# Kernel optimization log

Measured on AMD Instinct MI355X. Metric: run time of the kernel, lower is better.

The kernel has to match this reference:

```python
import jax, jax.numpy as jnp
import numpy as np

N_NODES = 100000
N_EDGES = 3200000
D_FEAT = 64
H_SIZE = 32
N_CLASSES = 10


def setup_inputs() -> dict:
    key = jax.random.key(0)
    ks = jax.random.split(key, 9)
    x = jax.random.normal(ks[0], (N_NODES, D_FEAT), dtype=jnp.float32)
    edge_index = jax.random.randint(ks[1], (2, N_EDGES), 0, N_NODES, dtype=jnp.int64)
    y = jax.random.randint(ks[2], (N_NODES,), 0, N_CLASSES, dtype=jnp.int64)
    s1 = 1.0 / np.sqrt(D_FEAT)
    s2 = 1.0 / np.sqrt(H_SIZE)
    W1_rel = jax.random.uniform(ks[3], (H_SIZE, D_FEAT), jnp.float32, -s1, s1)
    b1_rel = jax.random.uniform(ks[4], (H_SIZE,), jnp.float32, -s1, s1)
    W1_root = jax.random.uniform(ks[5], (H_SIZE, D_FEAT), jnp.float32, -s1, s1)
    W2_rel = jax.random.uniform(ks[6], (N_CLASSES, H_SIZE), jnp.float32, -s2, s2)
    b2_rel = jax.random.uniform(ks[7], (N_CLASSES,), jnp.float32, -s2, s2)
    W2_root = jax.random.uniform(ks[8], (N_CLASSES, H_SIZE), jnp.float32, -s2, s2)
    return {"x": x, "edge_index": edge_index, "y": y,
            "W1_rel": W1_rel, "b1_rel": b1_rel, "W1_root": W1_root,
            "W2_rel": W2_rel, "b2_rel": b2_rel, "W2_root": W2_root}


def _graph_conv(x, src, dst, W_rel, b_rel, W_root):
    # PyG GraphConv (aggr='add'): out_i = W_root x_i + b + W_rel * sum_{j: (j->i)} x_j
    agg = jax.ops.segment_sum(x[src], dst, num_segments=N_NODES)  # [N, d_in]
    return agg @ W_rel.T + b_rel + x @ W_root.T


def reference(x, edge_index, y, W1_rel, b1_rel, W1_root, W2_rel, b2_rel, W2_root):
    src, dst = edge_index[0], edge_index[1]
    h = jax.nn.relu(_graph_conv(x, src, dst, W1_rel, b1_rel, W1_root))  # [N, 32]
    logits = _graph_conv(h, src, dst, W2_rel, b2_rel, W2_root)          # [N, 10]
    logp = jax.nn.log_softmax(logits, axis=-1)
    loss = -jnp.mean(jnp.take_along_axis(logp, y[:, None], axis=-1)[:, 0])
    return loss
```

## Files before the change

### kernel.cpp

```cpp
#include <hip/hip_runtime.h>
#include <hip/hip_bf16.h>
#include <hip/hip_fp8.h>

#define D_FEAT 64
#define H_SIZE 32
#define N_CLASSES 10
#define NPB 256
#define MAXB 512
#define NCHUNK 256
#define BT 1024
#define NT 256

using short8 = __attribute__((ext_vector_type(8))) short;
using f32x4v = __attribute__((ext_vector_type(4))) float;

__device__ inline short f2bf(float f) {
    __hip_bfloat16 h = __float2bfloat16(f);
    return *reinterpret_cast<short*>(&h);
}


__global__ __launch_bounds__(NT) void dense1_mfma(
    const float* __restrict__ x, const float* __restrict__ W1_rel,
    const float* __restrict__ b1, const float* __restrict__ W1_root,
    unsigned* __restrict__ xr8, float* __restrict__ xroot, int n_nodes) {
    __shared__ unsigned short sW[64 * 72];
    __shared__ float sOut[64 * 65];
    __shared__ float sb[H_SIZE];
    int tid = threadIdx.x;
    for (int i = tid; i < 64 * 64; i += NT) {
        int n = i >> 6, k = i & 63;
        float w = (n < 32) ? W1_rel[n * 64 + k] : W1_root[(n - 32) * 64 + k];
        sW[n * 72 + k] = (unsigned short)f2bf(w);
    }
    if (tid < H_SIZE) sb[tid] = b1[tid];
    __syncthreads();

    int lane = tid & 63, wave = tid >> 6;
    int r16 = lane & 15, h = lane >> 4;

    short8 bf[4][2];
#pragma unroll
    for (int t = 0; t < 4; ++t)
#pragma unroll
        for (int s = 0; s < 2; ++s) {
            const unsigned short* p = &sW[(t * 16 + r16) * 72 + s * 32 + h * 8];
            bf[t][s] = *reinterpret_cast<const short8*>(p);
        }

    int nbase = blockIdx.x * 64 + wave * 16;
    int row = nbase + r16;
    int rowc = min(row, n_nodes - 1);

    short8 af[2];
#pragma unroll
    for (int s = 0; s < 2; ++s) {
        const float* px = x + (size_t)rowc * D_FEAT + s * 32 + h * 8;
        float4 lo = *reinterpret_cast<const float4*>(px);
        float4 hi = *reinterpret_cast<const float4*>(px + 4);
        short8 a;
        a[0] = f2bf(lo.x); a[1] = f2bf(lo.y); a[2] = f2bf(lo.z); a[3] = f2bf(lo.w);
        a[4] = f2bf(hi.x); a[5] = f2bf(hi.y); a[6] = f2bf(hi.z); a[7] = f2bf(hi.w);
        af[s] = a;
    }

    f32x4v acc[4] = {{0.f,0.f,0.f,0.f},{0.f,0.f,0.f,0.f},
                     {0.f,0.f,0.f,0.f},{0.f,0.f,0.f,0.f}};
#pragma unroll
    for (int t = 0; t < 4; ++t) {
        acc[t] = __builtin_amdgcn_mfma_f32_16x16x32_bf16(af[0], bf[t][0], acc[t], 0, 0, 0);
        acc[t] = __builtin_amdgcn_mfma_f32_16x16x32_bf16(af[1], bf[t][1], acc[t], 0, 0, 0);
    }
#pragma unroll
    for (int t = 0; t < 4; ++t)
#pragma unroll
        for (int r = 0; r < 4; ++r)
            sOut[(wave * 16 + h * 4 + r) * 65 + t * 16 + r16] = acc[t][r];
    __syncthreads();

    int nl = lane;
    int g = blockIdx.x * 64 + nl;
    if (g < n_nodes) {
        if (wave < 2) {
            unsigned w4[4];
#pragma unroll
            for (int q = 0; q < 4; ++q) {
                unsigned wd = 0;
#pragma unroll
                for (int b = 0; b < 4; ++b) {
                    float v = sOut[nl * 65 + wave * 16 + q * 4 + b];
                    __hip_fp8_e4m3 f8(v);
                    wd |= ((unsigned)f8.__x) << (8 * b);
                }
                w4[q] = wd;
            }
            *reinterpret_cast<uint4*>(&xr8[(size_t)g * 8 + wave * 4]) =
                make_uint4(w4[0], w4[1], w4[2], w4[3]);
        } else {
            int co = (wave - 2) * 16;
#pragma unroll
            for (int q = 0; q < 4; ++q) {
                float4 v;
                v.x = sOut[nl * 65 + 32 + co + q * 4 + 0] + sb[co + q * 4 + 0];
                v.y = sOut[nl * 65 + 32 + co + q * 4 + 1] + sb[co + q * 4 + 1];
                v.z = sOut[nl * 65 + 32 + co + q * 4 + 2] + sb[co + q * 4 + 2];
                v.w = sOut[nl * 65 + 32 + co + q * 4 + 3] + sb[co + q * 4 + 3];
                *reinterpret_cast<float4*>(&xroot[(size_t)g * 32 + co + q * 4]) = v;
            }
        }
    }
}


__global__ __launch_bounds__(BT) void bucket_count(
    const int* __restrict__ dst, int* __restrict__ counts,
    int n_edges, int nbuckets, int ept) {
    __shared__ int hist[MAXB];
    for (int i = threadIdx.x; i < nbuckets; i += BT) hist[i] = 0;
    __syncthreads();
    int beg = blockIdx.x * ept;
    int end = min(beg + ept, n_edges);
    for (int e = beg + threadIdx.x; e < end; e += BT)
        atomicAdd(&hist[dst[e] >> 8], 1);
    __syncthreads();
    for (int b = threadIdx.x; b < nbuckets; b += BT)
        counts[b * NCHUNK + blockIdx.x] = hist[b];
}

__global__ __launch_bounds__(NPB) void bucket_totals(
    const int* __restrict__ counts, int* __restrict__ totals) {
    int b = blockIdx.x, tid = threadIdx.x;
    int v = counts[b * NCHUNK + tid];
#pragma unroll
    for (int o = 32; o > 0; o >>= 1) v += __shfl_down(v, o, 64);
    __shared__ int part[NPB / 64];
    if ((tid & 63) == 0) part[tid >> 6] = v;
    __syncthreads();
    if (tid == 0) {
        int s = 0;
#pragma unroll
        for (int w = 0; w < NPB / 64; ++w) s += part[w];
        totals[b] = s;
    }
}

__global__ __launch_bounds__(MAXB) void scan_small(
    const int* __restrict__ totals, int* __restrict__ bbase, int nbuckets) {
    __shared__ int lds[MAXB];
    int tid = threadIdx.x;
    int v = (tid < nbuckets) ? totals[tid] : 0;
    lds[tid] = v;
    __syncthreads();
    for (int off = 1; off < MAXB; off <<= 1) {
        int t = (tid >= off) ? lds[tid - off] : 0;
        __syncthreads();
        lds[tid] += t;
        __syncthreads();
    }
    if (tid < nbuckets) bbase[tid] = lds[tid] - v;
}

__global__ __launch_bounds__(NPB) void scan_within(
    int* __restrict__ counts, const int* __restrict__ bbase) {
    __shared__ int lds[NPB];
    int b = blockIdx.x, tid = threadIdx.x;
    int v = counts[b * NCHUNK + tid];
    lds[tid] = v;
    __syncthreads();
    for (int off = 1; off < NPB; off <<= 1) {
        int t = (tid >= off) ? lds[tid - off] : 0;
        __syncthreads();
        lds[tid] += t;
        __syncthreads();
    }
    counts[b * NCHUNK + tid] = bbase[b] + lds[tid] - v;
}

__global__ __launch_bounds__(BT) void bucket_scatter(
    const int* __restrict__ src, const int* __restrict__ dst,
    const int* __restrict__ base, unsigned* __restrict__ packed,
    int n_edges, int nbuckets, int ept) {
    __shared__ int cur[MAXB];
    for (int b = threadIdx.x; b < nbuckets; b += BT)
        cur[b] = base[b * NCHUNK + blockIdx.x];
    __syncthreads();
    int beg = blockIdx.x * ept;
    int end = min(beg + ept, n_edges);
    for (int e = beg + threadIdx.x; e < end; e += BT) {
        int s = src[e], d = dst[e];
        int slot = atomicAdd(&cur[d >> 8], 1);
        packed[slot] = (unsigned)s | ((unsigned)(d & 255) << 24);
    }
}


__global__ __launch_bounds__(NPB) void csr_build(
    const unsigned* __restrict__ packed, const int* __restrict__ base,
    int* __restrict__ rowptr, int* __restrict__ csr,
    int n_nodes, int nbuckets, int n_edges) {
    __shared__ int cnt[NPB];
    __shared__ int cur[NPB];
    int b = blockIdx.x, tid = threadIdx.x;
    int pBeg = base[b * NCHUNK];
    int pEnd = (b + 1 < nbuckets) ? base[(b + 1) * NCHUNK] : n_edges;
    cnt[tid] = 0;
    __syncthreads();
    for (int i = pBeg + tid; i < pEnd; i += NPB)
        atomicAdd(&cnt[packed[i] >> 24], 1);
    __syncthreads();
    int v = cnt[tid];
    cur[tid] = v;
    __syncthreads();
    for (int off = 1; off < NPB; off <<= 1) {
        int t = (tid >= off) ? cur[tid - off] : 0;
        __syncthreads();
        cur[tid] += t;
        __syncthreads();
    }
    int gbase = pBeg + cur[tid] - v;
    int n = (b << 8) + tid;
    if (n < n_nodes) rowptr[n] = gbase;
    if (b == nbuckets - 1 && tid == 0) rowptr[n_nodes] = n_edges;
    cur[tid] = gbase;
    __syncthreads();
    for (int i = pBeg + tid; i < pEnd; i += NPB) {
        unsigned p = packed[i];
        int slot = atomicAdd(&cur[p >> 24], 1);
        csr[slot] = (int)(p & 0xFFFFFF);
    }
}


__global__ __launch_bounds__(NT) void gather1_kernel(
    const unsigned* __restrict__ xr8, const float* __restrict__ xroot,
    const int* __restrict__ rowptr, const int* __restrict__ csr,
    const float* __restrict__ W2_rel, const float* __restrict__ b2,
    const float* __restrict__ W2_root,
    __hip_bfloat16* __restrict__ h2, float* __restrict__ hroot, int n_nodes) {
    __shared__ float sWrelT[H_SIZE * 17];
    __shared__ float sWrootT[H_SIZE * 17];
    __shared__ float sb[16];
    __shared__ float sh[32][33];
    int tid = threadIdx.x;
    for (int i = tid; i < H_SIZE * 17; i += NT) { sWrelT[i] = 0.f; sWrootT[i] = 0.f; }
    __syncthreads();
    for (int i = tid; i < N_CLASSES * H_SIZE; i += NT) {
        int c = i >> 5, j = i & 31;
        sWrelT[j * 17 + c] = W2_rel[i];
        sWrootT[j * 17 + c] = W2_root[i];
    }
    if (tid < 16) sb[tid] = (tid < N_CLASSES) ? b2[tid] : 0.f;

    int t = blockIdx.x * NT + tid;
    int n = t >> 3, c2 = t & 7;
    float a0 = 0.f, a1 = 0.f, a2 = 0.f, a3 = 0.f;
    if (n < n_nodes) {
        int beg = rowptr[n], end = rowptr[n + 1];
        int nfull = (end - beg) & ~7;
        int i = beg;
        for (; i < beg + nfull; i += 8) {
            int e = csr[i + c2];
#pragma unroll
            for (int j = 0; j < 8; ++j) {
                int s = __shfl(e, j, 8);
                unsigned p = xr8[(size_t)s * 8 + c2];
                __hip_fp8_e4m3 f0, f1, f2, f3;
                f0.__x = (unsigned char)(p & 0xff);
                f1.__x = (unsigned char)((p >> 8) & 0xff);
                f2.__x = (unsigned char)((p >> 16) & 0xff);
                f3.__x = (unsigned char)(p >> 24);
                a0 += (float)f0; a1 += (float)f1; a2 += (float)f2; a3 += (float)f3;
            }
        }
        if (i < end) {
            int cnt = end - i;
            int e = csr[i + ((c2 < cnt) ? c2 : cnt - 1)];
#pragma unroll
            for (int j = 0; j < 8; ++j) {
                int s = __shfl(e, j, 8);
                unsigned p = xr8[(size_t)s * 8 + c2];
                if (j < cnt) {
                    __hip_fp8_e4m3 f0, f1, f2, f3;
                    f0.__x = (unsigned char)(p & 0xff);
                    f1.__x = (unsigned char)((p >> 8) & 0xff);
                    f2.__x = (unsigned char)((p >> 16) & 0xff);
                    f3.__x = (unsigned char)(p >> 24);
                    a0 += (float)f0; a1 += (float)f1; a2 += (float)f2; a3 += (float)f3;
                }
            }
        }
        float4 xr4 = *reinterpret_cast<const float4*>(&xroot[(size_t)n * 32 + c2 * 4]);
        a0 = fmaxf(a0 + xr4.x, 0.f);
        a1 = fmaxf(a1 + xr4.y, 0.f);
        a2 = fmaxf(a2 + xr4.z, 0.f);
        a3 = fmaxf(a3 + xr4.w, 0.f);
    }
    int nl = tid >> 3;
    sh[nl][c2 * 4 + 0] = a0;
    sh[nl][c2 * 4 + 1] = a1;
    sh[nl][c2 * 4 + 2] = a2;
    sh[nl][c2 * 4 + 3] = a3;
    __syncthreads();

#pragma unroll
    for (int pass = 0; pass < 2; ++pass) {
        int idx = pass * NT + tid;
        int nl2 = idx >> 4, c = idx & 15;
        int n2 = blockIdx.x * 32 + nl2;
        if (n2 < n_nodes) {
            float ar = 0.f, ao = 0.f;
#pragma unroll
            for (int j = 0; j < H_SIZE; ++j) {
                float hv = sh[nl2][j];
                ar += hv * sWrelT[j * 17 + c];
                ao += hv * sWrootT[j * 17 + c];
            }
            h2[(size_t)n2 * 16 + c] = __float2bfloat16(ar);
            hroot[(size_t)n2 * 16 + c] = ao + sb[c];
        }
    }
}


__global__ __launch_bounds__(NT) void gather2_loss_kernel(
    const unsigned* __restrict__ h2u,
    const float* __restrict__ hroot,
    const int* __restrict__ rowptr, const int* __restrict__ csr,
    const int* __restrict__ y, float* __restrict__ loss,
    int n_nodes, float invN) {
    int t = blockIdx.x * NT + threadIdx.x;
    int n = t >> 3, c2 = t & 7;
    int lane = threadIdx.x & 63;
    bool active = (n < n_nodes);

    float a0 = 0.f, a1 = 0.f;
    int yv = 0;
    if (active) {
        int beg = rowptr[n], end = rowptr[n + 1];
        int nfull = (end - beg) & ~7;
        int i = beg;
        for (; i < beg + nfull; i += 8) {
            int e = csr[i + c2];
#pragma unroll
            for (int j = 0; j < 8; ++j) {
                int s = __shfl(e, j, 8);
                unsigned p = h2u[(size_t)s * 8 + c2];
                a0 += __uint_as_float(p << 16);
                a1 += __uint_as_float(p & 0xFFFF0000u);
            }
        }
        if (i < end) {
            int cnt = end - i;
            int e = csr[i + ((c2 < cnt) ? c2 : cnt - 1)];
#pragma unroll
            for (int j = 0; j < 8; ++j) {
                int s = __shfl(e, j, 8);
                unsigned p = h2u[(size_t)s * 8 + c2];
                if (j < cnt) {
                    a0 += __uint_as_float(p << 16);
                    a1 += __uint_as_float(p & 0xFFFF0000u);
                }
            }
        }
        float2 hr = ((const float2*)hroot)[(size_t)n * 8 + c2];
        a0 += hr.x; a1 += hr.y;
        yv = y[n];
    }
    bool cv = active && (c2 < 5);
    float lm = cv ? fmaxf(a0, a1) : -INFINITY;
#pragma unroll
    for (int m = 1; m < 8; m <<= 1) lm = fmaxf(lm, __shfl_xor(lm, m, 64));
    float es = cv ? (expf(a0 - lm) + expf(a1 - lm)) : 0.f;
#pragma unroll
    for (int m = 1; m < 8; m <<= 1) es += __shfl_xor(es, m, 64);
    int srcl = (lane & ~7) + (yv >> 1);
    float ly0 = __shfl(a0, srcl, 64);
    float ly1 = __shfl(a1, srcl, 64);
    float ly = (yv & 1) ? ly1 : ly0;
    float contrib = (active && c2 == 0) ? (lm + logf(es) - ly) * invN : 0.f;

#pragma unroll
    for (int o = 32; o > 0; o >>= 1) contrib += __shfl_down(contrib, o, 64);
    __shared__ float part[NT / 64];
    if (lane == 0) part[threadIdx.x >> 6] = contrib;
    __syncthreads();
    if (threadIdx.x == 0) {
        float v = 0.f;
#pragma unroll
        for (int w = 0; w < NT / 64; ++w) v += part[w];
        atomicAdd(loss, v);
    }
}


extern "C" void kernel_launch(void* const* d_in, const int* in_sizes, int n_in,
                              void* d_out, int out_size, void* d_ws, size_t ws_size,
                              hipStream_t stream) {
    const float* x       = (const float*)d_in[0];
    const int*   ei      = (const int*)d_in[1];
    const int*   y       = (const int*)d_in[2];
    const float* W1_rel  = (const float*)d_in[3];
    const float* b1_rel  = (const float*)d_in[4];
    const float* W1_root = (const float*)d_in[5];
    const float* W2_rel  = (const float*)d_in[6];
    const float* b2_rel  = (const float*)d_in[7];
    const float* W2_root = (const float*)d_in[8];
    float* loss = (float*)d_out;

    const int n_nodes = in_sizes[0] / D_FEAT;
    const int n_edges = in_sizes[1] / 2;
    const int* src = ei;
    const int* dst = ei + n_edges;

    const int nbuckets = (n_nodes + NPB - 1) / NPB;
    const int M = nbuckets * NCHUNK;
    const int ept = (n_edges + NCHUNK - 1) / NCHUNK;

    size_t off = 0;
    auto alloc = [&](size_t bytes) {
        void* p = (char*)d_ws + off;
        off = (off + bytes + 255) & ~(size_t)255;
        return p;
    };
    int*            counts = (int*)alloc((size_t)(M + 1) * 4);
    int*            totals = (int*)alloc((size_t)MAXB * 4);
    int*            bbase  = (int*)alloc((size_t)MAXB * 4);
    unsigned*       packed = (unsigned*)alloc((size_t)n_edges * 4);
    int*            rowptr = (int*)alloc((size_t)(n_nodes + 1) * 4);
    int*            csr    = (int*)alloc((size_t)n_edges * 4);
    unsigned*       xr8    = (unsigned*)alloc((size_t)n_nodes * 32);
    float*          xroot  = (float*)alloc((size_t)n_nodes * H_SIZE * 4);
    __hip_bfloat16* h2     = (__hip_bfloat16*)alloc((size_t)n_nodes * 16 * 2);
    float*          hroot  = (float*)alloc((size_t)n_nodes * 16 * 4);

    dense1_mfma<<<(n_nodes + 63) / 64, NT, 0, stream>>>(
        x, W1_rel, b1_rel, W1_root, xr8, xroot, n_nodes);

    bucket_count<<<NCHUNK, BT, 0, stream>>>(dst, counts, n_edges, nbuckets, ept);
    bucket_totals<<<nbuckets, NPB, 0, stream>>>(counts, totals);
    scan_small<<<1, MAXB, 0, stream>>>(totals, bbase, nbuckets);
    scan_within<<<nbuckets, NPB, 0, stream>>>(counts, bbase);
    bucket_scatter<<<NCHUNK, BT, 0, stream>>>(src, dst, counts, packed,
                                              n_edges, nbuckets, ept);
    csr_build<<<nbuckets, NPB, 0, stream>>>(packed, counts, rowptr, csr,
                                            n_nodes, nbuckets, n_edges);

    gather1_kernel<<<(n_nodes + 31) / 32, NT, 0, stream>>>(
        xr8, xroot, rowptr, csr, W2_rel, b2_rel, W2_root, h2, hroot, n_nodes);

    hipMemsetAsync(loss, 0, sizeof(float), stream);
    gather2_loss_kernel<<<(n_nodes + 31) / 32, NT, 0, stream>>>(
        (const unsigned*)h2, hroot, rowptr, csr, y, loss,
        n_nodes, 1.f / (float)n_nodes);
}
```

Before: 163.9 us.

## Use two lanes per node with 16-byte vector gathers in both aggregation kernels

Both gather kernels change from 8 lanes per node with 4-byte loads to 2 lanes per node with uint4 (16-byte) loads. Each lane now holds 16 fp8 or 8 bf16 accumulators, and each block covers 128 nodes instead of 32. This cuts the number of memory instructions and shuffles per edge and reduces the wasted padding on tail edges. The cost is more registers per thread and less lane parallelism per node, so more latency must be hidden by having more nodes in flight; the log-softmax reduction is rewritten to match the new lane layout.

After: 161.8 us. No clear change (-1.2%).

```diff
diff --git a/kernel.cpp b/kernel.cpp
--- a/kernel.cpp
+++ b/kernel.cpp
@@ -18,6 +18,20 @@
     __hip_bfloat16 h = __float2bfloat16(f);
     return *reinterpret_cast<short*>(&h);
 }
+
+#define F8(u, s) ({ __hip_fp8_e4m3 _f; _f.__x = (unsigned char)(((u) >> (s)) & 0xff); (float)_f; })
+
+#define ACC16(p) do { \
+    a[0]  += F8((p).x, 0);  a[1]  += F8((p).x, 8);  a[2]  += F8((p).x, 16); a[3]  += F8((p).x, 24); \
+    a[4]  += F8((p).y, 0);  a[5]  += F8((p).y, 8);  a[6]  += F8((p).y, 16); a[7]  += F8((p).y, 24); \
+    a[8]  += F8((p).z, 0);  a[9]  += F8((p).z, 8);  a[10] += F8((p).z, 16); a[11] += F8((p).z, 24); \
+    a[12] += F8((p).w, 0);  a[13] += F8((p).w, 8);  a[14] += F8((p).w, 16); a[15] += F8((p).w, 24); } while (0)
+
+#define ACC8(p) do { \
+    a[0] += __uint_as_float((p).x << 16); a[1] += __uint_as_float((p).x & 0xFFFF0000u); \
+    a[2] += __uint_as_float((p).y << 16); a[3] += __uint_as_float((p).y & 0xFFFF0000u); \
+    a[4] += __uint_as_float((p).z << 16); a[5] += __uint_as_float((p).z & 0xFFFF0000u); \
+    a[6] += __uint_as_float((p).w << 16); a[7] += __uint_as_float((p).w & 0xFFFF0000u); } while (0)
 
 
 __global__ __launch_bounds__(NT) void dense1_mfma(
@@ -232,7 +246,8 @@
 
 
 __global__ __launch_bounds__(NT) void gather1_kernel(
-    const unsigned* __restrict__ xr8, const float* __restrict__ xroot,
+    const uint4* __restrict__ xr8v,
+    const float* __restrict__ xroot,
     const int* __restrict__ rowptr, const int* __restrict__ csr,
     const float* __restrict__ W2_rel, const float* __restrict__ b2,
     const float* __restrict__ W2_root,
@@ -240,7 +255,7 @@
     __shared__ float sWrelT[H_SIZE * 17];
     __shared__ float sWrootT[H_SIZE * 17];
     __shared__ float sb[16];
-    __shared__ float sh[32][33];
+    __shared__ float sh[128][33];
     int tid = threadIdx.x;
     for (int i = tid; i < H_SIZE * 17; i += NT) { sWrelT[i] = 0.f; sWrootT[i] = 0.f; }
     __syncthreads();
@@ -252,61 +267,54 @@
     if (tid < 16) sb[tid] = (tid < N_CLASSES) ? b2[tid] : 0.f;
 
     int t = blockIdx.x * NT + tid;
-    int n = t >> 3, c2 = t & 7;
-    float a0 = 0.f, a1 = 0.f, a2 = 0.f, a3 = 0.f;
+    int n = t >> 1, c1 = t & 1;
+    float a[16] = {0.f,0.f,0.f,0.f,0.f,0.f,0.f,0.f,
+                   0.f,0.f,0.f,0.f,0.f,0.f,0.f,0.f};
     if (n < n_nodes) {
         int beg = rowptr[n], end = rowptr[n + 1];
-        int nfull = (end - beg) & ~7;
         int i = beg;
-        for (; i < beg + nfull; i += 8) {
-            int e = csr[i + c2];
-#pragma unroll
-            for (int j = 0; j < 8; ++j) {
-                int s = __shfl(e, j, 8);
-                unsigned p = xr8[(size_t)s * 8 + c2];
-                __hip_fp8_e4m3 f0, f1, f2, f3;
-                f0.__x = (unsigned char)(p & 0xff);
-                f1.__x = (unsigned char)((p >> 8) & 0xff);
-                f2.__x = (unsigned char)((p >> 16) & 0xff);
-                f3.__x = (unsigned char)(p >> 24);
-                a0 += (float)f0; a1 += (float)f1; a2 += (float)f2; a3 += (float)f3;
-            }
+        for (; i + 4 <= end; i += 4) {
+            int e0 = csr[i + c1];
+            int e1 = csr[i + 2 + c1];
+            uint4 p0 = xr8v[(size_t)__shfl(e0, 0, 2) * 2 + c1];
+            uint4 p1 = xr8v[(size_t)__shfl(e0, 1, 2) * 2 + c1];
+            uint4 p2 = xr8v[(size_t)__shfl(e1, 0, 2) * 2 + c1];
+            uint4 p3 = xr8v[(size_t)__shfl(e1, 1, 2) * 2 + c1];
+            ACC16(p0); ACC16(p1); ACC16(p2); ACC16(p3);
+        }
+        if (i + 2 <= end) {
+            int e0 = csr[i + c1];
+            uint4 p0 = xr8v[(size_t)__shfl(e0, 0, 2) * 2 + c1];
+            uint4 p1 = xr8v[(size_t)__shfl(e0, 1, 2) * 2 + c1];
+            ACC16(p0); ACC16(p1);
+            i += 2;
         }
         if (i < end) {
-            int cnt = end - i;
-            int e = csr[i + ((c2 < cnt) ? c2 : cnt - 1)];
-#pragma unroll
-            for (int j = 0; j < 8; ++j) {
-                int s = __shfl(e, j, 8);
-                unsigned p = xr8[(size_t)s * 8 + c2];
-                if (j < cnt) {
-                    __hip_fp8_e4m3 f0, f1, f2, f3;
-                    f0.__x = (unsigned char)(p & 0xff);
-                    f1.__x = (unsigned char)((p >> 8) & 0xff);
-                    f2.__x = (unsigned char)((p >> 16) & 0xff);
-                    f3.__x = (unsigned char)(p >> 24);
-                    a0 += (float)f0; a1 += (float)f1; a2 += (float)f2; a3 += (float)f3;
-                }
-            }
-        }
-        float4 xr4 = *reinterpret_cast<const float4*>(&xroot[(size_t)n * 32 + c2 * 4]);
-        a0 = fmaxf(a0 + xr4.x, 0.f);
-        a1 = fmaxf(a1 + xr4.y, 0.f);
-        a2 = fmaxf(a2 + xr4.z, 0.f);
-        a3 = fmaxf(a3 + xr4.w, 0.f);
-    }
-    int nl = tid >> 3;
-    sh[nl][c2 * 4 + 0] = a0;
-    sh[nl][c2 * 4 + 1] = a1;
-    sh[nl][c2 * 4 + 2] = a2;
-    sh[nl][c2 * 4 + 3] = a3;
-    __syncthreads();
-
-#pragma unroll
-    for (int pass = 0; pass < 2; ++pass) {
+            int e = csr[i];
+            uint4 p = xr8v[(size_t)e * 2 + c1];
+            ACC16(p);
+        }
+        const float4* xr4 = reinterpret_cast<const float4*>(
+            xroot + (size_t)n * 32 + c1 * 16);
+#pragma unroll
+        for (int q = 0; q < 4; ++q) {
+            float4 v = xr4[q];
+            a[q * 4 + 0] = fmaxf(a[q * 4 + 0] + v.x, 0.f);
+            a[q * 4 + 1] = fmaxf(a[q * 4 + 1] + v.y, 0.f);
+            a[q * 4 + 2] = fmaxf(a[q * 4 + 2] + v.z, 0.f);
+            a[q * 4 + 3] = fmaxf(a[q * 4 + 3] + v.w, 0.f);
+        }
+    }
+    int nl = tid >> 1;
+#pragma unroll
+    for (int j = 0; j < 16; ++j) sh[nl][c1 * 16 + j] = a[j];
+    __syncthreads();
+
+#pragma unroll
+    for (int pass = 0; pass < 8; ++pass) {
         int idx = pass * NT + tid;
         int nl2 = idx >> 4, c = idx & 15;
-        int n2 = blockIdx.x * 32 + nl2;
+        int n2 = blockIdx.x * 128 + nl2;
         if (n2 < n_nodes) {
             float ar = 0.f, ao = 0.f;
 #pragma unroll
@@ -323,61 +331,70 @@
 
 
 __global__ __launch_bounds__(NT) void gather2_loss_kernel(
-    const unsigned* __restrict__ h2u,
+    const uint4* __restrict__ h2v,
     const float* __restrict__ hroot,
     const int* __restrict__ rowptr, const int* __restrict__ csr,
     const int* __restrict__ y, float* __restrict__ loss,
     int n_nodes, float invN) {
     int t = blockIdx.x * NT + threadIdx.x;
-    int n = t >> 3, c2 = t & 7;
+    int n = t >> 1, c1 = t & 1;
     int lane = threadIdx.x & 63;
     bool active = (n < n_nodes);
 
-    float a0 = 0.f, a1 = 0.f;
+    float a[8] = {0.f,0.f,0.f,0.f,0.f,0.f,0.f,0.f};
     int yv = 0;
     if (active) {
         int beg = rowptr[n], end = rowptr[n + 1];
-        int nfull = (end - beg) & ~7;
         int i = beg;
-        for (; i < beg + nfull; i += 8) {
-            int e = csr[i + c2];
-#pragma unroll
-            for (int j = 0; j < 8; ++j) {
-                int s = __shfl(e, j, 8);
-                unsigned p = h2u[(size_t)s * 8 + c2];
-                a0 += __uint_as_float(p << 16);
-                a1 += __uint_as_float(p & 0xFFFF0000u);
-            }
+        for (; i + 4 <= end; i += 4) {
+            int e0 = csr[i + c1];
+            int e1 = csr[i + 2 + c1];
+            uint4 p0 = h2v[(size_t)__shfl(e0, 0, 2) * 2 + c1];
+            uint4 p1 = h2v[(size_t)__shfl(e0, 1, 2) * 2 + c1];
+            uint4 p2 = h2v[(size_t)__shfl(e1, 0, 2) * 2 + c1];
+            uint4 p3 = h2v[(size_t)__shfl(e1, 1, 2) * 2 + c1];
+            ACC8(p0); ACC8(p1); ACC8(p2); ACC8(p3);
+        }
+        if (i + 2 <= end) {
+            int e0 = csr[i + c1];
+            uint4 p0 = h2v[(size_t)__shfl(e0, 0, 2) * 2 + c1];
+            uint4 p1 = h2v[(size_t)__shfl(e0, 1, 2) * 2 + c1];
+            ACC8(p0); ACC8(p1);
+            i += 2;
         }
         if (i < end) {
-            int cnt = end - i;
-            int e = csr[i + ((c2 < cnt) ? c2 : cnt - 1)];
-#pragma unroll
-            for (int j = 0; j < 8; ++j) {
-                int s = __shfl(e, j, 8);
-                unsigned p = h2u[(size_t)s * 8 + c2];
-                if (j < cnt) {
-                    a0 += __uint_as_float(p << 16);
-                    a1 += __uint_as_float(p & 0xFFFF0000u);
-                }
-            }
-        }
-        float2 hr = ((const float2*)hroot)[(size_t)n * 8 + c2];
-        a0 += hr.x; a1 += hr.y;
+            int e = csr[i];
+            uint4 p = h2v[(size_t)e * 2 + c1];
+            ACC8(p);
+        }
+        const float4* hr4 = reinterpret_cast<const float4*>(
+            hroot + (size_t)n * 16 + c1 * 8);
+        float4 h0 = hr4[0], h1 = hr4[1];
+        a[0] += h0.x; a[1] += h0.y; a[2] += h0.z; a[3] += h0.w;
+        a[4] += h1.x; a[5] += h1.y; a[6] += h1.z; a[7] += h1.w;
         yv = y[n];
     }
-    bool cv = active && (c2 < 5);
-    float lm = cv ? fmaxf(a0, a1) : -INFINITY;
-#pragma unroll
-    for (int m = 1; m < 8; m <<= 1) lm = fmaxf(lm, __shfl_xor(lm, m, 64));
-    float es = cv ? (expf(a0 - lm) + expf(a1 - lm)) : 0.f;
-#pragma unroll
-    for (int m = 1; m < 8; m <<= 1) es += __shfl_xor(es, m, 64);
-    int srcl = (lane & ~7) + (yv >> 1);
-    float ly0 = __shfl(a0, srcl, 64);
-    float ly1 = __shfl(a1, srcl, 64);
-    float ly = (yv & 1) ? ly1 : ly0;
-    float contrib = (active && c2 == 0) ? (lm + logf(es) - ly) * invN : 0.f;
+    bool full = active && (c1 == 0);
+    float m = -INFINITY;
+#pragma unroll
+    for (int j = 0; j < 8; ++j) {
+        bool v = (j < 2) ? active : full;
+        m = fmaxf(m, v ? a[j] : -INFINITY);
+    }
+    m = fmaxf(m, __shfl_xor(m, 1, 64));
+    float es = 0.f;
+#pragma unroll
+    for (int j = 0; j < 8; ++j) {
+        bool v = (j < 2) ? active : full;
+        es += v ? expf(a[j] - m) : 0.f;
+    }
+    es += __shfl_xor(es, 1, 64);
+    int yl = yv & 7;
+    float lyc = 0.f;
+#pragma unroll
+    for (int j = 0; j < 8; ++j) lyc = (j == yl) ? a[j] : lyc;
+    float ly = __shfl(lyc, (lane & ~1) + (yv >> 3), 64);
+    float contrib = (active && c1 == 0) ? (m + logf(es) - ly) * invN : 0.f;
 
 #pragma unroll
     for (int o = 32; o > 0; o >>= 1) contrib += __shfl_down(contrib, o, 64);
@@ -445,11 +462,12 @@
     csr_build<<<nbuckets, NPB, 0, stream>>>(packed, counts, rowptr, csr,
                                             n_nodes, nbuckets, n_edges);
 
-    gather1_kernel<<<(n_nodes + 31) / 32, NT, 0, stream>>>(
-        xr8, xroot, rowptr, csr, W2_rel, b2_rel, W2_root, h2, hroot, n_nodes);
+    gather1_kernel<<<(n_nodes + 127) / 128, NT, 0, stream>>>(
+        (const uint4*)xr8, xroot, rowptr, csr,
+        W2_rel, b2_rel, W2_root, h2, hroot, n_nodes);
 
     hipMemsetAsync(loss, 0, sizeof(float), stream);
-    gather2_loss_kernel<<<(n_nodes + 31) / 32, NT, 0, stream>>>(
-        (const unsigned*)h2, hroot, rowptr, csr, y, loss,
+    gather2_loss_kernel<<<(n_nodes + 127) / 128, NT, 0, stream>>>(
+        (const uint4*)h2, hroot, rowptr, csr, y, loss,
         n_nodes, 1.f / (float)n_nodes);
 }
```
